# Performance work log

Measured on AMD Instinct MI355X. Metric: run time of the kernel, lower is better.

The kernel has to match this reference:

```python
import jax, jax.numpy as jnp
import numpy as np

HIDDEN = 64
HALF = 32
VOCAB = 64
B, L = 256, 2048


def _l2norm(x):
    # matches torch F.normalize(dim=-1, eps=1e-12)
    return x / jnp.maximum(jnp.linalg.norm(x, axis=-1, keepdims=True), 1e-12)


def setup_inputs() -> dict:
    key = jax.random.key(0)
    ks = jax.random.split(key, 16)
    s = 0.02
    return {
        "seq": jax.random.randint(ks[0], (B, L), 0, VOCAB),
        "embed": jax.random.normal(ks[1], (VOCAB, HIDDEN), jnp.float32) * s,
        "W1": jax.random.normal(ks[2], (2 * HIDDEN, HIDDEN), jnp.float32) * s,
        "b1": jnp.zeros((2 * HIDDEN,), jnp.float32),
        "W2": jax.random.normal(ks[3], (HIDDEN, 2 * HIDDEN), jnp.float32) * s,
        "b2": jnp.zeros((HIDDEN,), jnp.float32),
        "ln_g": jnp.ones((HIDDEN,), jnp.float32),
        "ln_b": jnp.zeros((HIDDEN,), jnp.float32),
        "Ws": jax.random.normal(ks[4], (HALF, HIDDEN), jnp.float32) * s,
        "bs": jnp.zeros((HALF,), jnp.float32),
        "We": jax.random.normal(ks[5], (HALF, HIDDEN), jnp.float32) * s,
        "be": jnp.zeros((HALF,), jnp.float32),
        "Wrp": jax.random.normal(ks[6], (HIDDEN, 2 * HALF), jnp.float32) * s,
        "brp": jnp.zeros((HIDDEN,), jnp.float32),
        "Wo": jax.random.normal(ks[7], (VOCAB, HIDDEN), jnp.float32) * s,
        "bo": jnp.zeros((VOCAB,), jnp.float32),
    }


def reference(seq, embed, W1, b1, W2, b2, ln_g, ln_b, Ws, bs, We, be, Wrp, brp, Wo, bo):
    # Encoder: embed -> LayerNorm(h + FF(h))
    h0 = embed[seq]                                     # [B,L,H]
    ff = jnp.maximum(h0 @ W1.T + b1, 0.0) @ W2.T + b2
    x = h0 + ff
    mu = x.mean(-1, keepdims=True)
    var = x.var(-1, keepdims=True)
    h = (x - mu) / jnp.sqrt(var + 1e-5) * ln_g + ln_b   # [B,L,H]

    Bn, Ln, _ = h.shape
    half = Ws.shape[0]
    hs_all = h @ Ws.T + bs                              # [B,L,half]
    he_all = h @ We.T + be

    # sequential delta-rule memory writes over t = 0 .. L-2
    hs_seq = jnp.swapaxes(hs_all[:, :-1], 0, 1)         # [L-1,B,half]
    he_seq = jnp.swapaxes(he_all[:, :-1], 0, 1)
    scales = (jnp.arange(1, Ln) / Ln).astype(h.dtype)   # (t+1)/L
    M0 = jnp.zeros((Bn, half, half), h.dtype)

    def step(carry, inp):
        M_s, M_e = carry
        hs, he, sc = inp
        ks_ = _l2norm(hs)
        ke_ = _l2norm(he)
        vps = jnp.einsum('bij,bj->bi', M_s, ks_)
        vpe = jnp.einsum('bij,bj->bi', M_e, ke_)
        M_s = M_s + (hs - vps)[:, :, None] * ks_[:, None, :]
        M_e = M_e + sc * (he - vpe)[:, :, None] * ke_[:, None, :]
        return (M_s, M_e), None

    (M_s, M_e), _ = jax.lax.scan(step, (M0, M0), (hs_seq, he_seq, scales))

    # read with last-position query
    qs = _l2norm(hs_all[:, -1])
    qe = _l2norm(he_all[:, -1])
    rs = jnp.einsum('bij,bj->bi', M_s, qs)
    re = jnp.einsum('bij,bj->bi', M_e, qe)
    r = jnp.concatenate([rs, re], axis=-1)              # [B, 2*half]
    return (r @ Wrp.T + brp) @ Wo.T + bo                # [B, vocab]
```

## Files before the change

kernel.cpp:

```cpp
#include <hip/hip_runtime.h>

#define HIDDEN 64
#define HALFD  32
#define VOCAB  64
#define BATCH  256
#define SEQLEN 2048

#define RLF(v, sl) __int_as_float(__builtin_amdgcn_readlane(__float_as_int(v), (sl)))
#define RLI(v, sl) __builtin_amdgcn_readlane((v), (sl))
#define SWZF(v, j) __int_as_float(__builtin_amdgcn_ds_swizzle(__float_as_int(v), ((j) << 5)))
#define GIX(j,m) (((j)==0?0:(j)==1?7:(j)==2?13:(j)==3?18:(j)==4?22:(j)==5?25:27) + (m) - (j) - 1)
#define OM(m) (((m)*((m)+1))>>1)

__global__ __launch_bounds__(256) void vocab_kernel(
    const float* __restrict__ embed, const float* __restrict__ W1, const float* __restrict__ b1,
    const float* __restrict__ W2, const float* __restrict__ b2,
    const float* __restrict__ ln_g, const float* __restrict__ ln_b,
    const float* __restrict__ Ws, const float* __restrict__ bs,
    const float* __restrict__ We, const float* __restrict__ be,
    float* __restrict__ ws)
{
    const int v = blockIdx.x;
    const int tid = threadIdx.x;

    __shared__ float e_s[64];
    __shared__ float W1_s[128][65];
    __shared__ float W2_s[64][129];
    __shared__ float Wse_s[64][65];
    __shared__ float a1_s[128];
    __shared__ float h_s[64];

    if (tid < 64) e_s[tid] = embed[v * 64 + tid];
    {
        const float4* src = (const float4*)W1;
        for (int i = tid; i < 2048; i += 256) {
            float4 x4 = src[i];
            const int e = i << 2, r = e >> 6, c = e & 63;
            W1_s[r][c] = x4.x; W1_s[r][c+1] = x4.y; W1_s[r][c+2] = x4.z; W1_s[r][c+3] = x4.w;
        }
    }
    __syncthreads();

    if (tid < 128) {
        float p0 = b1[tid], p1 = 0.f, p2 = 0.f, p3 = 0.f;
        #pragma unroll
        for (int m = 0; m < 64; m += 4) {
            p0 = fmaf(e_s[m],   W1_s[tid][m],   p0);
            p1 = fmaf(e_s[m+1], W1_s[tid][m+1], p1);
            p2 = fmaf(e_s[m+2], W1_s[tid][m+2], p2);
            p3 = fmaf(e_s[m+3], W1_s[tid][m+3], p3);
        }
        a1_s[tid] = fmaxf((p0 + p1) + (p2 + p3), 0.0f);
    } else {
        const float4* src = (const float4*)W2;
        for (int i = tid - 128; i < 2048; i += 128) {
            float4 x4 = src[i];
            const int e = i << 2, r = e >> 7, c = e & 127;
            W2_s[r][c] = x4.x; W2_s[r][c+1] = x4.y; W2_s[r][c+2] = x4.z; W2_s[r][c+3] = x4.w;
        }
    }
    __syncthreads();

    if (tid < 64) {
        float f0 = b2[tid], f1 = 0.f, f2 = 0.f, f3 = 0.f;
        #pragma unroll
        for (int m = 0; m < 128; m += 4) {
            f0 = fmaf(a1_s[m],   W2_s[tid][m],   f0);
            f1 = fmaf(a1_s[m+1], W2_s[tid][m+1], f1);
            f2 = fmaf(a1_s[m+2], W2_s[tid][m+2], f2);
            f3 = fmaf(a1_s[m+3], W2_s[tid][m+3], f3);
        }
        float x = e_s[tid] + ((f0 + f1) + (f2 + f3));
        float s = x, s2 = x * x;
        #pragma unroll
        for (int off = 32; off >= 1; off >>= 1) {
            s  += __shfl_xor(s,  off, 64);
            s2 += __shfl_xor(s2, off, 64);
        }
        float mu  = s * (1.0f / 64.0f);
        float var = s2 * (1.0f / 64.0f) - mu * mu;
        h_s[tid] = (x - mu) * rsqrtf(var + 1e-5f) * ln_g[tid] + ln_b[tid];
    } else if (tid < 192) {
        const int t2 = tid - 64;
        const float4* s1 = (const float4*)Ws;
        const float4* s2 = (const float4*)We;
        for (int i = t2; i < 512; i += 128) {
            float4 x4 = s1[i];
            const int e = i << 2, r = e >> 6, c = e & 63;
            Wse_s[r][c] = x4.x; Wse_s[r][c+1] = x4.y; Wse_s[r][c+2] = x4.z; Wse_s[r][c+3] = x4.w;
        }
        for (int i = t2; i < 512; i += 128) {
            float4 x4 = s2[i];
            const int e = i << 2, r = e >> 6, c = e & 63;
            Wse_s[32+r][c] = x4.x; Wse_s[32+r][c+1] = x4.y; Wse_s[32+r][c+2] = x4.z; Wse_s[32+r][c+3] = x4.w;
        }
    }
    __syncthreads();

    if (tid < 64) {
        const int j = tid & 31;
        const bool is_s = tid < 32;
        float c0 = is_s ? bs[j] : be[j];
        float c1 = 0.f, c2 = 0.f, c3 = 0.f;
        #pragma unroll
        for (int m = 0; m < 64; m += 4) {
            c0 = fmaf(h_s[m],   Wse_s[tid][m],   c0);
            c1 = fmaf(h_s[m+1], Wse_s[tid][m+1], c1);
            c2 = fmaf(h_s[m+2], Wse_s[tid][m+2], c2);
            c3 = fmaf(h_s[m+3], Wse_s[tid][m+3], c3);
        }
        float acc = (c0 + c1) + (c2 + c3);

        float n2 = acc * acc;
        #pragma unroll
        for (int off = 16; off >= 1; off >>= 1) n2 += __shfl_xor(n2, off, 64);
        float norm = sqrtf(n2);
        float kn = acc / fmaxf(norm, 1e-12f);

        const int base = v * 32 + j;
        if (is_s) { ws[base]        = kn; ws[4096 + base] = acc; }
        else      { ws[2048 + base] = kn; ws[6144 + base] = acc; }
    }
}

__global__ __launch_bounds__(256) void gram_kernel(float* __restrict__ ws)
{
    const int w   = blockIdx.x & 1;
    const int seg = blockIdx.x >> 1;
    const int tid = threadIdx.x;
    __shared__ float k_s[64][33];
    const float* kb = ws + w * 2048;
    for (int i = tid; i < 2048; i += 256) k_s[i >> 5][i & 31] = kb[i];
    __syncthreads();
    const int a  = seg * 16 + (tid >> 4);
    const int b0 = (tid & 15) << 2;
    float* Gw = ws + 8192 + w * 4096 + a * 64;
    #pragma unroll
    for (int bb = 0; bb < 4; ++bb) {
        const int bcol = b0 + bb;
        float acc0 = 0.f, acc1 = 0.f;
        #pragma unroll
        for (int m = 0; m < 32; m += 2) {
            acc0 = fmaf(k_s[a][m],     k_s[bcol][m],     acc0);
            acc1 = fmaf(k_s[a][m + 1], k_s[bcol][m + 1], acc1);
        }
        Gw[bcol] = acc0 + acc1;
    }
}

static __device__ __forceinline__ void build_wpack(
    const int* tj, float fb, float invL, bool is_e, bool is_last, float* Wp,
    const float* __restrict__ Gg)
{
    float f[8];
    #pragma unroll
    for (int j = 0; j < 8; ++j) f[j] = is_e ? (fb + (float)j * invL) : 1.0f;
    if (is_last) f[7] = 0.0f;

    float g[28];
    #pragma unroll
    for (int j = 0; j < 7; ++j)
        #pragma unroll
        for (int m = j + 1; m < 8; ++m) g[GIX(j, m)] = Gg[tj[j] * 64 + tj[m]];

    #pragma unroll
    for (int m = 0; m < 8; ++m) {
        float col[8];
        col[m] = f[m];
        #pragma unroll
        for (int j = 6; j >= 0; --j) {
            if (j < m) {
                float acc = 0.0f;
                #pragma unroll
                for (int p = 1; p < 8; ++p)
                    if (p > j && p <= m) acc = fmaf(g[GIX(j, p)], col[p], acc);
                col[j] = -f[j] * acc;
            }
        }
        #pragma unroll
        for (int j = 0; j < 8; ++j)
            if (j <= m) Wp[OM(m) + j] = col[j];
    }
}

struct Chunk {
    int   tokv;
    int   tk[8];
    float grow[8];
    float R[8];
    float braw;
    float bp[8];
};

__global__ __launch_bounds__(128) void scan_kernel(
    const int* __restrict__ seq, const float* __restrict__ ws,
    const float* __restrict__ Wrp, const float* __restrict__ brp,
    const float* __restrict__ Wo, const float* __restrict__ bo,
    float* __restrict__ out)
{
    const int b    = blockIdx.x;
    const int tid  = threadIdx.x;
    const int w    = tid >> 6;
    const int lane = tid & 63;
    const int l7   = lane & 7;
    const bool is_e = (w == 1);

    __shared__ __align__(16) float Wlds[2][256][8][8];
    __shared__ __align__(16) int   toklds[SEQLEN];
    __shared__ float wacc_s[2][64];
    __shared__ float r_s[64];
    __shared__ float t1_s[64];

    const float* Gg = ws + 8192 + w * 4096;
    const int*   sq = seq + b * SEQLEN;

    {
        const int4* sq4 = (const int4*)sq;
        int4* tl = (int4*)toklds;
        #pragma unroll
        for (int i = 0; i < 4; ++i) tl[tid + i * 128] = sq4[tid + i * 128];
    }
    __syncthreads();

    {
        const float invL = 1.0f / (float)SEQLEN;
        #pragma unroll
        for (int qq = 0; qq < 4; ++qq) {
            const int c = lane + (qq << 6);
            int tj[8];
            #pragma unroll
            for (int j = 0; j < 8; ++j) tj[j] = toklds[c * 8 + j];
            float Wp[36];
            build_wpack(tj, (float)(8 * c + 1) * invL, invL, is_e, c == 255, Wp, Gg);
            const int cx = c & 7;
            #pragma unroll
            for (int i = 0; i < 8; ++i) {
                float r[8];
                #pragma unroll
                for (int m = 0; m < 8; ++m) r[m] = (m >= i) ? Wp[OM(m) + i] : 0.0f;
                float4* dst = (float4*)&Wlds[w][c][i ^ cx][0];
                dst[0] = make_float4(r[0], r[1], r[2], r[3]);
                dst[1] = make_float4(r[4], r[5], r[6], r[7]);
            }
        }
    }
    __syncthreads();

    Chunk A, B;
    float u, wacc0 = 0.0f, wacc1 = 0.0f;
    float sp0, sp1, sp2, sp3, sp4, sp5, sp6, sp7;

    A.tokv = sq[2040 + l7];
    B.tokv = sq[2032 + l7];
    int tv2 = sq[2024 + l7];
    #pragma unroll
    for (int j = 0; j < 8; ++j) A.tk[j] = RLI(A.tokv, j);
    #pragma unroll
    for (int j = 0; j < 8; ++j) A.grow[j] = Gg[A.tk[j] * 64 + lane];
    {
        const float4* rp = (const float4*)&Wlds[w][255][l7 ^ 7][0];
        float4 lo = rp[0], hi = rp[1];
        A.R[0] = lo.x; A.R[1] = lo.y; A.R[2] = lo.z; A.R[3] = lo.w;
        A.R[4] = hi.x; A.R[5] = hi.y; A.R[6] = hi.z; A.R[7] = hi.w;
    }
    u = Gg[A.tk[7] * 64 + lane];
    A.braw = __shfl(u, A.tokv, 64);
    B.braw = __shfl(u, B.tokv, 64);
    #pragma unroll
    for (int j = 0; j < 8; ++j) {
        A.bp[j] = 0.0f;
        B.bp[j] = __shfl(A.grow[j], B.tokv, 64);
    }
    sp0 = sp1 = sp2 = sp3 = sp4 = sp5 = sp6 = sp7 = 0.0f;

    auto body = [&](Chunk& cur, Chunk& nxt, int c) {
        const int cm1 = (c > 0) ? c - 1 : 0;
        const int cm3 = (c > 2) ? c - 3 : 0;

        float c01 = fmaf(cur.bp[1], sp1, cur.bp[0] * sp0);
        float c23 = fmaf(cur.bp[3], sp3, cur.bp[2] * sp2);
        float c45 = fmaf(cur.bp[5], sp5, cur.bp[4] * sp4);
        float c67 = fmaf(cur.bp[7], sp7, cur.bp[6] * sp6);
        float tl = cur.braw - ((c01 + c23) + (c45 + c67));

        float t0 = SWZF(tl, 0), t1 = SWZF(tl, 1), t2 = SWZF(tl, 2), t3 = SWZF(tl, 3);
        float t4 = SWZF(tl, 4), t5 = SWZF(tl, 5), t6 = SWZF(tl, 6), t7 = SWZF(tl, 7);

        #pragma unroll
        for (int j = 0; j < 8; ++j) nxt.bp[j] = __shfl(cur.grow[j], nxt.tokv, 64);
        #pragma unroll
        for (int j = 0; j < 8; ++j) nxt.tk[j] = RLI(nxt.tokv, j);
        #pragma unroll
        for (int j = 0; j < 8; ++j) nxt.grow[j] = Gg[nxt.tk[j] * 64 + lane];
        {
            const float4* rp = (const float4*)&Wlds[w][cm1][l7 ^ (cm1 & 7)][0];
            float4 lo = rp[0], hi = rp[1];
            nxt.R[0] = lo.x; nxt.R[1] = lo.y; nxt.R[2] = lo.z; nxt.R[3] = lo.w;
            nxt.R[4] = hi.x; nxt.R[5] = hi.y; nxt.R[6] = hi.z; nxt.R[7] = hi.w;
        }
        int tv3 = sq[cm3 * 8 + l7];

        const float* R = cur.R;
        float a0 = fmaf(R[1], t1, R[0] * t0);
        float a1 = fmaf(R[3], t3, R[2] * t2);
        float a2 = fmaf(R[5], t5, R[4] * t4);
        float a3 = fmaf(R[7], t7, R[6] * t6);
        float sd = (a0 + a1) + (a2 + a3);

        float s0 = SWZF(sd, 0), s1 = SWZF(sd, 1), s2 = SWZF(sd, 2), s3 = SWZF(sd, 3);
        float s4 = SWZF(sd, 4), s5 = SWZF(sd, 5), s6 = SWZF(sd, 6), s7 = SWZF(sd, 7);

        float dA = fmaf(cur.grow[0], s0, fmaf(cur.grow[1], s1, fmaf(cur.grow[2], s2, cur.grow[3] * s3)));
        float dB = fmaf(cur.grow[4], s4, fmaf(cur.grow[5], s5, fmaf(cur.grow[6], s6, cur.grow[7] * s7)));
        u -= (dA + dB);
        cur.braw = __shfl(u, tv2, 64);

        wacc0 += (lane == cur.tk[0]) ? s0 : 0.0f;
        wacc1 += (lane == cur.tk[1]) ? s1 : 0.0f;
        wacc0 += (lane == cur.tk[2]) ? s2 : 0.0f;
        wacc1 += (lane == cur.tk[3]) ? s3 : 0.0f;
        wacc0 += (lane == cur.tk[4]) ? s4 : 0.0f;
        wacc1 += (lane == cur.tk[5]) ? s5 : 0.0f;
        wacc0 += (lane == cur.tk[6]) ? s6 : 0.0f;
        wacc1 += (lane == cur.tk[7]) ? s7 : 0.0f;

        cur.tokv = tv2; tv2 = tv3;
        sp0 = s0; sp1 = s1; sp2 = s2; sp3 = s3;
        sp4 = s4; sp5 = s5; sp6 = s6; sp7 = s7;
    };

    for (int c = 255; c >= 1; c -= 2) {
        body(A, B, c);
        body(B, A, c - 1);
    }

    wacc_s[w][lane] = wacc0 + wacc1;
    __syncthreads();

    if (tid < 64) {
        const int w2  = tid >> 5;
        const int rho = tid & 31;
        const float* vv = ws + 4096 + w2 * 2048;
        const float* wa = &wacc_s[w2][0];
        float acc = 0.0f;
        #pragma unroll 8
        for (int tok = 0; tok < 64; ++tok) acc = fmaf(wa[tok], vv[tok * 32 + rho], acc);
        r_s[tid] = acc;
    }
    __syncthreads();

    if (tid < 64) {
        float acc = brp[tid];
        #pragma unroll 8
        for (int m = 0; m < 64; ++m) acc = fmaf(Wrp[tid * 64 + m], r_s[m], acc);
        t1_s[tid] = acc;
    }
    __syncthreads();
    if (tid < 64) {
        float acc = bo[tid];
        #pragma unroll 8
        for (int m = 0; m < 64; ++m) acc = fmaf(Wo[tid * 64 + m], t1_s[m], acc);
        out[b * 64 + tid] = acc;
    }
}

extern "C" void kernel_launch(void* const* d_in, const int* in_sizes, int n_in,
                              void* d_out, int out_size, void* d_ws, size_t ws_size,
                              hipStream_t stream)
{
    const int*   seq   = (const int*)  d_in[0];
    const float* embed = (const float*)d_in[1];
    const float* W1    = (const float*)d_in[2];
    const float* b1    = (const float*)d_in[3];
    const float* W2    = (const float*)d_in[4];
    const float* b2    = (const float*)d_in[5];
    const float* ln_g  = (const float*)d_in[6];
    const float* ln_b  = (const float*)d_in[7];
    const float* Ws    = (const float*)d_in[8];
    const float* bs    = (const float*)d_in[9];
    const float* We    = (const float*)d_in[10];
    const float* be    = (const float*)d_in[11];
    const float* Wrp   = (const float*)d_in[12];
    const float* brp   = (const float*)d_in[13];
    const float* Wo    = (const float*)d_in[14];
    const float* bo    = (const float*)d_in[15];
    float* ws  = (float*)d_ws;
    float* out = (float*)d_out;

    hipLaunchKernelGGL(vocab_kernel, dim3(VOCAB), dim3(256), 0, stream,
                       embed, W1, b1, W2, b2, ln_g, ln_b, Ws, bs, We, be, ws);
    hipLaunchKernelGGL(gram_kernel, dim3(8), dim3(256), 0, stream, ws);
    hipLaunchKernelGGL(scan_kernel, dim3(BATCH), dim3(128), 0, stream,
                       seq, ws, Wrp, brp, Wo, bo, out);
}
```

Measured before the change: 193.7 us.

## Process two 8-token chunks per scan iteration with 16-token bundles

```diff
diff --git a/kernel.cpp b/kernel.cpp
--- a/kernel.cpp
+++ b/kernel.cpp
@@ -9,6 +9,7 @@
 #define RLF(v, sl) __int_as_float(__builtin_amdgcn_readlane(__float_as_int(v), (sl)))
 #define RLI(v, sl) __builtin_amdgcn_readlane((v), (sl))
 #define SWZF(v, j) __int_as_float(__builtin_amdgcn_ds_swizzle(__float_as_int(v), ((j) << 5)))
+#define SWZE(v)    __int_as_float(__builtin_amdgcn_ds_swizzle(__float_as_int(v), 0x0007))
 #define GIX(j,m) (((j)==0?0:(j)==1?7:(j)==2?13:(j)==3?18:(j)==4?22:(j)==5?25:27) + (m) - (j) - 1)
 #define OM(m) (((m)*((m)+1))>>1)
 
@@ -183,13 +184,15 @@
     }
 }
 
-struct Chunk {
+struct C16 {
     int   tokv;
-    int   tk[8];
-    float grow[8];
-    float R[8];
+    int   tk[16];
+    float grow[16];
+    float R1[8];
+    float R2[8];
     float braw;
-    float bp[8];
+    float bpp[16];
+    float gx[8];
 };
 
 __global__ __launch_bounds__(128) void scan_kernel(
@@ -203,6 +206,7 @@
     const int w    = tid >> 6;
     const int lane = tid & 63;
     const int l7   = lane & 7;
+    const int l15  = lane & 15;
     const bool is_e = (w == 1);
 
     __shared__ __align__(16) float Wlds[2][256][8][8];
@@ -216,9 +220,9 @@
 
     {
         const int4* sq4 = (const int4*)sq;
-        int4* tl = (int4*)toklds;
-        #pragma unroll
-        for (int i = 0; i < 4; ++i) tl[tid + i * 128] = sq4[tid + i * 128];
+        int4* tl4 = (int4*)toklds;
+        #pragma unroll
+        for (int i = 0; i < 4; ++i) tl4[tid + i * 128] = sq4[tid + i * 128];
     }
     __syncthreads();
 
@@ -246,95 +250,147 @@
     }
     __syncthreads();
 
-    Chunk A, B;
-    float u, wacc0 = 0.0f, wacc1 = 0.0f;
-    float sp0, sp1, sp2, sp3, sp4, sp5, sp6, sp7;
-
-    A.tokv = sq[2040 + l7];
-    B.tokv = sq[2032 + l7];
-    int tv2 = sq[2024 + l7];
-    #pragma unroll
-    for (int j = 0; j < 8; ++j) A.tk[j] = RLI(A.tokv, j);
-    #pragma unroll
-    for (int j = 0; j < 8; ++j) A.grow[j] = Gg[A.tk[j] * 64 + lane];
+    C16 A, B;
+    float u, wc0 = 0.f, wc1 = 0.f, wc2 = 0.f, wc3 = 0.f;
+    float sp[16];
+    int tv2;
+
+    A.tokv = sq[127 * 16 + l15];
+    B.tokv = sq[126 * 16 + l15];
+    tv2    = sq[125 * 16 + l15];
+    #pragma unroll
+    for (int j = 0; j < 16; ++j) A.tk[j] = RLI(A.tokv, j);
+    #pragma unroll
+    for (int j = 0; j < 16; ++j) A.grow[j] = Gg[A.tk[j] * 64 + lane];
     {
         const float4* rp = (const float4*)&Wlds[w][255][l7 ^ 7][0];
         float4 lo = rp[0], hi = rp[1];
-        A.R[0] = lo.x; A.R[1] = lo.y; A.R[2] = lo.z; A.R[3] = lo.w;
-        A.R[4] = hi.x; A.R[5] = hi.y; A.R[6] = hi.z; A.R[7] = hi.w;
-    }
-    u = Gg[A.tk[7] * 64 + lane];
+        A.R1[0]=lo.x; A.R1[1]=lo.y; A.R1[2]=lo.z; A.R1[3]=lo.w;
+        A.R1[4]=hi.x; A.R1[5]=hi.y; A.R1[6]=hi.z; A.R1[7]=hi.w;
+        const float4* rq = (const float4*)&Wlds[w][254][l7 ^ 6][0];
+        float4 lo2 = rq[0], hi2 = rq[1];
+        A.R2[0]=lo2.x; A.R2[1]=lo2.y; A.R2[2]=lo2.z; A.R2[3]=lo2.w;
+        A.R2[4]=hi2.x; A.R2[5]=hi2.y; A.R2[6]=hi2.z; A.R2[7]=hi2.w;
+    }
+    u = Gg[A.tk[15] * 64 + lane];
     A.braw = __shfl(u, A.tokv, 64);
     B.braw = __shfl(u, B.tokv, 64);
     #pragma unroll
-    for (int j = 0; j < 8; ++j) {
-        A.bp[j] = 0.0f;
-        B.bp[j] = __shfl(A.grow[j], B.tokv, 64);
-    }
-    sp0 = sp1 = sp2 = sp3 = sp4 = sp5 = sp6 = sp7 = 0.0f;
-
-    auto body = [&](Chunk& cur, Chunk& nxt, int c) {
-        const int cm1 = (c > 0) ? c - 1 : 0;
-        const int cm3 = (c > 2) ? c - 3 : 0;
-
-        float c01 = fmaf(cur.bp[1], sp1, cur.bp[0] * sp0);
-        float c23 = fmaf(cur.bp[3], sp3, cur.bp[2] * sp2);
-        float c45 = fmaf(cur.bp[5], sp5, cur.bp[4] * sp4);
-        float c67 = fmaf(cur.bp[7], sp7, cur.bp[6] * sp6);
-        float tl = cur.braw - ((c01 + c23) + (c45 + c67));
-
-        float t0 = SWZF(tl, 0), t1 = SWZF(tl, 1), t2 = SWZF(tl, 2), t3 = SWZF(tl, 3);
-        float t4 = SWZF(tl, 4), t5 = SWZF(tl, 5), t6 = SWZF(tl, 6), t7 = SWZF(tl, 7);
-
-        #pragma unroll
-        for (int j = 0; j < 8; ++j) nxt.bp[j] = __shfl(cur.grow[j], nxt.tokv, 64);
-        #pragma unroll
-        for (int j = 0; j < 8; ++j) nxt.tk[j] = RLI(nxt.tokv, j);
-        #pragma unroll
-        for (int j = 0; j < 8; ++j) nxt.grow[j] = Gg[nxt.tk[j] * 64 + lane];
+    for (int j = 0; j < 16; ++j) A.bpp[j] = 0.0f;
+    {
+        int addrE = __shfl(A.tokv, l7, 64);
+        #pragma unroll
+        for (int j = 0; j < 8; ++j) A.gx[j] = Gg[A.tk[8 + j] * 64 + addrE];
+    }
+    #pragma unroll
+    for (int j = 0; j < 16; ++j) sp[j] = 0.0f;
+
+    auto body16 = [&](C16& cur, C16& nxt, int C) {
+        const int cm1 = (C > 0) ? C - 1 : 0;
+        const int cm3 = (C > 2) ? C - 3 : 0;
+
+        float q0 = fmaf(cur.bpp[1],  sp[1],  cur.bpp[0]  * sp[0]);
+        float q1 = fmaf(cur.bpp[3],  sp[3],  cur.bpp[2]  * sp[2]);
+        float q2 = fmaf(cur.bpp[5],  sp[5],  cur.bpp[4]  * sp[4]);
+        float q3 = fmaf(cur.bpp[7],  sp[7],  cur.bpp[6]  * sp[6]);
+        float q4 = fmaf(cur.bpp[9],  sp[9],  cur.bpp[8]  * sp[8]);
+        float q5 = fmaf(cur.bpp[11], sp[11], cur.bpp[10] * sp[10]);
+        float q6 = fmaf(cur.bpp[13], sp[13], cur.bpp[12] * sp[12]);
+        float q7 = fmaf(cur.bpp[15], sp[15], cur.bpp[14] * sp[14]);
+        float tl = cur.braw - (((q0 + q1) + (q2 + q3)) + ((q4 + q5) + (q6 + q7)));
+
+        float tL0 = SWZF(tl, 8),  tL1 = SWZF(tl, 9),  tL2 = SWZF(tl, 10), tL3 = SWZF(tl, 11);
+        float tL4 = SWZF(tl, 12), tL5 = SWZF(tl, 13), tL6 = SWZF(tl, 14), tL7 = SWZF(tl, 15);
+        float tE  = SWZE(tl);
+
+        #pragma unroll
+        for (int j = 0; j < 16; ++j) nxt.bpp[j] = __shfl(cur.grow[j], nxt.tokv, 64);
+        #pragma unroll
+        for (int j = 0; j < 16; ++j) nxt.tk[j] = RLI(nxt.tokv, j);
+        #pragma unroll
+        for (int j = 0; j < 16; ++j) nxt.grow[j] = Gg[nxt.tk[j] * 64 + lane];
         {
-            const float4* rp = (const float4*)&Wlds[w][cm1][l7 ^ (cm1 & 7)][0];
+            const int c8a = 2 * cm1 + 1, c8b = 2 * cm1;
+            const float4* rp = (const float4*)&Wlds[w][c8a][l7 ^ (c8a & 7)][0];
             float4 lo = rp[0], hi = rp[1];
-            nxt.R[0] = lo.x; nxt.R[1] = lo.y; nxt.R[2] = lo.z; nxt.R[3] = lo.w;
-            nxt.R[4] = hi.x; nxt.R[5] = hi.y; nxt.R[6] = hi.z; nxt.R[7] = hi.w;
-        }
-        int tv3 = sq[cm3 * 8 + l7];
-
-        const float* R = cur.R;
-        float a0 = fmaf(R[1], t1, R[0] * t0);
-        float a1 = fmaf(R[3], t3, R[2] * t2);
-        float a2 = fmaf(R[5], t5, R[4] * t4);
-        float a3 = fmaf(R[7], t7, R[6] * t6);
-        float sd = (a0 + a1) + (a2 + a3);
-
-        float s0 = SWZF(sd, 0), s1 = SWZF(sd, 1), s2 = SWZF(sd, 2), s3 = SWZF(sd, 3);
-        float s4 = SWZF(sd, 4), s5 = SWZF(sd, 5), s6 = SWZF(sd, 6), s7 = SWZF(sd, 7);
-
-        float dA = fmaf(cur.grow[0], s0, fmaf(cur.grow[1], s1, fmaf(cur.grow[2], s2, cur.grow[3] * s3)));
-        float dB = fmaf(cur.grow[4], s4, fmaf(cur.grow[5], s5, fmaf(cur.grow[6], s6, cur.grow[7] * s7)));
-        u -= (dA + dB);
+            nxt.R1[0]=lo.x; nxt.R1[1]=lo.y; nxt.R1[2]=lo.z; nxt.R1[3]=lo.w;
+            nxt.R1[4]=hi.x; nxt.R1[5]=hi.y; nxt.R1[6]=hi.z; nxt.R1[7]=hi.w;
+            const float4* rq = (const float4*)&Wlds[w][c8b][l7 ^ (c8b & 7)][0];
+            float4 lo2 = rq[0], hi2 = rq[1];
+            nxt.R2[0]=lo2.x; nxt.R2[1]=lo2.y; nxt.R2[2]=lo2.z; nxt.R2[3]=lo2.w;
+            nxt.R2[4]=hi2.x; nxt.R2[5]=hi2.y; nxt.R2[6]=hi2.z; nxt.R2[7]=hi2.w;
+        }
+        {
+            int addrE = __shfl(nxt.tokv, l7, 64);
+            #pragma unroll
+            for (int j = 0; j < 8; ++j) nxt.gx[j] = Gg[nxt.tk[8 + j] * 64 + addrE];
+        }
+        int tv3 = sq[cm3 * 16 + l15];
+
+        const float* R1 = cur.R1;
+        float a0 = fmaf(R1[1], tL1, R1[0] * tL0);
+        float a1 = fmaf(R1[3], tL3, R1[2] * tL2);
+        float a2 = fmaf(R1[5], tL5, R1[4] * tL4);
+        float a3 = fmaf(R1[7], tL7, R1[6] * tL6);
+        float sd1 = (a0 + a1) + (a2 + a3);
+        float s10 = SWZF(sd1, 0), s11 = SWZF(sd1, 1), s12 = SWZF(sd1, 2), s13 = SWZF(sd1, 3);
+        float s14 = SWZF(sd1, 4), s15 = SWZF(sd1, 5), s16 = SWZF(sd1, 6), s17 = SWZF(sd1, 7);
+
+        const float* gx = cur.gx;
+        float b0 = fmaf(gx[1], s11, gx[0] * s10);
+        float b1 = fmaf(gx[3], s13, gx[2] * s12);
+        float b2 = fmaf(gx[5], s15, gx[4] * s14);
+        float b3 = fmaf(gx[7], s17, gx[6] * s16);
+        float tpl = tE - ((b0 + b1) + (b2 + b3));
+        float tP0 = SWZF(tpl, 0), tP1 = SWZF(tpl, 1), tP2 = SWZF(tpl, 2), tP3 = SWZF(tpl, 3);
+        float tP4 = SWZF(tpl, 4), tP5 = SWZF(tpl, 5), tP6 = SWZF(tpl, 6), tP7 = SWZF(tpl, 7);
+
+        const float* R2 = cur.R2;
+        float e0 = fmaf(R2[1], tP1, R2[0] * tP0);
+        float e1 = fmaf(R2[3], tP3, R2[2] * tP2);
+        float e2 = fmaf(R2[5], tP5, R2[4] * tP4);
+        float e3 = fmaf(R2[7], tP7, R2[6] * tP6);
+        float sd2 = (e0 + e1) + (e2 + e3);
+        float s20 = SWZF(sd2, 0), s21 = SWZF(sd2, 1), s22 = SWZF(sd2, 2), s23 = SWZF(sd2, 3);
+        float s24 = SWZF(sd2, 4), s25 = SWZF(sd2, 5), s26 = SWZF(sd2, 6), s27 = SWZF(sd2, 7);
+
+        float dA = fmaf(cur.grow[8],  s10, fmaf(cur.grow[9],  s11, fmaf(cur.grow[10], s12, cur.grow[11] * s13)));
+        float dB = fmaf(cur.grow[12], s14, fmaf(cur.grow[13], s15, fmaf(cur.grow[14], s16, cur.grow[15] * s17)));
+        float dC = fmaf(cur.grow[0],  s20, fmaf(cur.grow[1],  s21, fmaf(cur.grow[2],  s22, cur.grow[3]  * s23)));
+        float dD = fmaf(cur.grow[4],  s24, fmaf(cur.grow[5],  s25, fmaf(cur.grow[6],  s26, cur.grow[7]  * s27)));
+        u -= (dA + dB) + (dC + dD);
         cur.braw = __shfl(u, tv2, 64);
 
-        wacc0 += (lane == cur.tk[0]) ? s0 : 0.0f;
-        wacc1 += (lane == cur.tk[1]) ? s1 : 0.0f;
-        wacc0 += (lane == cur.tk[2]) ? s2 : 0.0f;
-        wacc1 += (lane == cur.tk[3]) ? s3 : 0.0f;
-        wacc0 += (lane == cur.tk[4]) ? s4 : 0.0f;
-        wacc1 += (lane == cur.tk[5]) ? s5 : 0.0f;
-        wacc0 += (lane == cur.tk[6]) ? s6 : 0.0f;
-        wacc1 += (lane == cur.tk[7]) ? s7 : 0.0f;
+        wc0 += (lane == cur.tk[8])  ? s10 : 0.0f;
+        wc1 += (lane == cur.tk[9])  ? s11 : 0.0f;
+        wc2 += (lane == cur.tk[10]) ? s12 : 0.0f;
+        wc3 += (lane == cur.tk[11]) ? s13 : 0.0f;
+        wc0 += (lane == cur.tk[12]) ? s14 : 0.0f;
+        wc1 += (lane == cur.tk[13]) ? s15 : 0.0f;
+        wc2 += (lane == cur.tk[14]) ? s16 : 0.0f;
+        wc3 += (lane == cur.tk[15]) ? s17 : 0.0f;
+        wc0 += (lane == cur.tk[0])  ? s20 : 0.0f;
+        wc1 += (lane == cur.tk[1])  ? s21 : 0.0f;
+        wc2 += (lane == cur.tk[2])  ? s22 : 0.0f;
+        wc3 += (lane == cur.tk[3])  ? s23 : 0.0f;
+        wc0 += (lane == cur.tk[4])  ? s24 : 0.0f;
+        wc1 += (lane == cur.tk[5])  ? s25 : 0.0f;
+        wc2 += (lane == cur.tk[6])  ? s26 : 0.0f;
+        wc3 += (lane == cur.tk[7])  ? s27 : 0.0f;
 
         cur.tokv = tv2; tv2 = tv3;
-        sp0 = s0; sp1 = s1; sp2 = s2; sp3 = s3;
-        sp4 = s4; sp5 = s5; sp6 = s6; sp7 = s7;
+        sp[8]  = s10; sp[9]  = s11; sp[10] = s12; sp[11] = s13;
+        sp[12] = s14; sp[13] = s15; sp[14] = s16; sp[15] = s17;
+        sp[0]  = s20; sp[1]  = s21; sp[2]  = s22; sp[3]  = s23;
+        sp[4]  = s24; sp[5]  = s25; sp[6]  = s26; sp[7]  = s27;
     };
 
-    for (int c = 255; c >= 1; c -= 2) {
-        body(A, B, c);
-        body(B, A, c - 1);
-    }
-
-    wacc_s[w][lane] = wacc0 + wacc1;
+    for (int C = 127; C >= 1; C -= 2) {
+        body16(A, B, C);
+        body16(B, A, C - 1);
+    }
+
+    wacc_s[w][lane] = (wc0 + wc1) + (wc2 + wc3);
     __syncthreads();
 
     if (tid < 64) {
```

Result: slower. 207.1 us (+7.0%).
